# Performance work log

Measured on AMD Instinct MI355X. Metric: run time of the kernel, lower is better.

Reference implementation:

```python
import jax, jax.numpy as jnp
import numpy as np

B, T, D, H = 4, 2048, 1024, 16
DK = D // H
LN_EPS = 1e-5


def setup_inputs() -> dict:
    key = jax.random.key(0)
    ks = jax.random.split(key, 12)
    s = 1.0 / np.sqrt(D)
    inp = {
        'x': jax.random.normal(ks[0], (B, T, D), jnp.float32),
        'Wq': jax.random.normal(ks[1], (D, D), jnp.float32) * s,
        'bq': jnp.zeros((D,), jnp.float32),
        'Wk': jax.random.normal(ks[2], (D, D), jnp.float32) * s,
        'bk': jnp.zeros((D,), jnp.float32),
        'Wv': jax.random.normal(ks[3], (D, D), jnp.float32) * s,
        'bv': jnp.zeros((D,), jnp.float32),
        'Wo': jax.random.normal(ks[4], (D, D), jnp.float32) * s,
        'bo': jnp.zeros((D,), jnp.float32),
        'ln_g': jnp.ones((D,), jnp.float32),
        'ln_b': jnp.zeros((D,), jnp.float32),
    }
    return inp


def reference(x, Wq, bq, Wk, bk, Wv, bv, Wo, bo, ln_g, ln_b):
    b, t, d = x.shape
    scale = jnp.sqrt(jnp.asarray(DK, x.dtype))
    # QKV projections -> [b, h, t, dk]
    q = (x @ Wq + bq).reshape(b, t, H, DK).transpose(0, 2, 1, 3)
    k = (x @ Wk + bk).reshape(b, t, H, DK).transpose(0, 2, 1, 3)
    v = (x @ Wv + bv).reshape(b, t, H, DK).transpose(0, 2, 1, 3)
    scores = jnp.einsum('bhqd,bhkd->bhqk', q, k) / scale  # [b,h,t,t]
    mask = jnp.tril(jnp.ones((t, t), x.dtype))[None, None]  # [1,1,t,t]
    neg = jnp.finfo(x.dtype).min
    scores = jnp.where(mask == 0, neg, scores)
    attn = jax.nn.softmax(scores, axis=-1)
    # mask-renormalize (as in the torch module)
    attn = attn * mask
    denom = attn.sum(-1, keepdims=True)
    attn = jnp.where(denom > 0, attn / denom, jnp.zeros_like(attn))
    ctx = jnp.einsum('bhqk,bhkd->bhqd', attn, v)  # [b,h,t,dk]
    ctx = ctx.transpose(0, 2, 1, 3).reshape(b, t, d)
    out = ctx @ Wo + bo
    y = out + x  # residual
    mu = y.mean(-1, keepdims=True)
    var = ((y - mu) ** 2).mean(-1, keepdims=True)
    return (y - mu) / jnp.sqrt(var + LN_EPS) * ln_g + ln_b
```

## Files before the change

### kernel.cpp

```cpp
#include <hip/hip_runtime.h>


using u16 = unsigned short;
using u32 = unsigned int;
typedef _Float16 f16x8 __attribute__((ext_vector_type(8)));
typedef __fp16 h16x2 __attribute__((ext_vector_type(2)));
typedef float f32x4 __attribute__((ext_vector_type(4)));
typedef unsigned short u16x8 __attribute__((ext_vector_type(8)));
typedef unsigned short u16x4 __attribute__((ext_vector_type(4)));

template <bool B> struct BoolTag { static constexpr bool v = B; };

__device__ inline u16 f2h_bits(float f) {
    _Float16 h = (_Float16)f;
    return __builtin_bit_cast(u16, h);
}
__device__ inline float h2f(u16 u) {
    return (float)__builtin_bit_cast(_Float16, u);
}

__device__ __forceinline__ void gload16(const void* g, void* l) {
    __builtin_amdgcn_global_load_lds(
        (const __attribute__((address_space(1))) void*)g,
        (__attribute__((address_space(3))) void*)l, 16, 0, 0);
}

__global__ __launch_bounds__(256) void convert_kernel(
    const float* __restrict__ x, u16* __restrict__ xb,
    const float* __restrict__ W0, const float* __restrict__ W1,
    const float* __restrict__ W2, const float* __restrict__ W3,
    u16* __restrict__ Wt) {
    __shared__ float ts[64][68];
    const int bid = blockIdx.x, tid = threadIdx.x;
    if (bid < 4096) {
        size_t i = ((size_t)bid * 256 + tid) * 8;
        float4 a = *(const float4*)(x + i);
        float4 b = *(const float4*)(x + i + 4);
        u16x8 o;
        o[0] = f2h_bits(a.x); o[1] = f2h_bits(a.y); o[2] = f2h_bits(a.z); o[3] = f2h_bits(a.w);
        o[4] = f2h_bits(b.x); o[5] = f2h_bits(b.y); o[6] = f2h_bits(b.z); o[7] = f2h_bits(b.w);
        *(u16x8*)(xb + i) = o;
        return;
    }
    const int wb = bid - 4096;
    const int z = wb >> 8, rem = wb & 255;
    const float* W = z == 0 ? W0 : (z == 1 ? W1 : (z == 2 ? W2 : W3));
    u16* Wo = Wt + (size_t)z * 1048576;
    const int k0 = (rem >> 4) * 64, n0 = (rem & 15) * 64;
    const int rr = tid >> 3, c = tid & 7;
#pragma unroll
    for (int p = 0; p < 2; p++) {
        int k = p * 32 + rr;
        float4 u = *(const float4*)(W + (size_t)(k0 + k) * 1024 + n0 + c * 8);
        float4 w = *(const float4*)(W + (size_t)(k0 + k) * 1024 + n0 + c * 8 + 4);
        *(float4*)&ts[k][c * 8] = u;
        *(float4*)&ts[k][c * 8 + 4] = w;
    }
    __syncthreads();
#pragma unroll
    for (int p = 0; p < 2; p++) {
        int n = p * 32 + rr;
        u16 o[8];
#pragma unroll
        for (int j = 0; j < 8; j++) o[j] = f2h_bits(ts[c * 8 + j][n]);
        *(u16x8*)(Wo + (size_t)(n0 + n) * 1024 + k0 + c * 8) = *(u16x8*)o;
    }
}

template <int MODE>
__global__ __launch_bounds__(512) void gemm256_kernel(
    const u16* __restrict__ A, const u16* __restrict__ Wt,
    const float* __restrict__ b0, const float* __restrict__ b1,
    const float* __restrict__ b2, u16* __restrict__ qo, u16* __restrict__ ko,
    u16* __restrict__ vt) {
    constexpr int NBY = (MODE == 0) ? 12 : 4;
    __shared__ u16 As[3][128 * 64];
    __shared__ u16 Bs[3][256 * 64];

    const int bid = blockIdx.x;
    const int cpx = (MODE == 0) ? 96 : 32;
    const int swz = (bid & 7) * cpx + (bid >> 3);
    const int bx = swz / NBY, by = swz % NBY;
    const size_t row0 = (size_t)bx * 128;
    const size_t col0 = (size_t)by * 256;

    const int tid = threadIdx.x, lane = tid & 63;
    const int wid = tid >> 6, wm = wid >> 2, wn = wid & 3;
    const int l15 = lane & 15, lg = lane >> 4;
    const int rr = tid >> 3, c8 = tid & 7;
    const int scw = (c8 ^ (rr & 7)) * 8;

    f32x4 acc[4][4] = {};

    auto stage_half = [&](int kt, u16* dA, u16* dB, int h) {
        const int k0 = kt * 64;
        if (h == 0) {
            gload16(A + (row0 + rr) * 1024 + k0 + scw, dA + tid * 8);
            gload16(Wt + (col0 + rr) * 1024 + k0 + scw, dB + tid * 8);
            gload16(Wt + (col0 + 64 + rr) * 1024 + k0 + scw, dB + (512 + tid) * 8);
        } else {
            gload16(A + (row0 + 64 + rr) * 1024 + k0 + scw, dA + (512 + tid) * 8);
            gload16(Wt + (col0 + 128 + rr) * 1024 + k0 + scw, dB + (1024 + tid) * 8);
            gload16(Wt + (col0 + 192 + rr) * 1024 + k0 + scw, dB + (1536 + tid) * 8);
        }
    };

    auto ldops = [&](const u16* bA, const u16* bB, int kcv, f16x8* Af, f16x8* Bf) {
        const int swo = ((kcv * 4 + lg) ^ (l15 & 7)) * 8;
#pragma unroll
        for (int n = 0; n < 4; n++)
            Bf[n] = *(const f16x8*)(bB + (wn * 64 + n * 16 + l15) * 64 + swo);
#pragma unroll
        for (int m = 0; m < 4; m++)
            Af[m] = *(const f16x8*)(bA + (wm * 64 + m * 16 + l15) * 64 + swo);
    };

    auto domfma = [&](const f16x8* Af, const f16x8* Bf) {
        __builtin_amdgcn_s_setprio(1);
#pragma unroll
        for (int m = 0; m < 4; m++)
#pragma unroll
            for (int n = 0; n < 4; n++)
                acc[m][n] = __builtin_amdgcn_mfma_f32_16x16x32_f16(
                    Af[m], Bf[n], acc[m][n], 0, 0, 0);
        __builtin_amdgcn_s_setprio(0);
    };

    u16 *pA = &As[0][0], *pnA = &As[1][0], *ppA = &As[2][0];
    u16 *pB = &Bs[0][0], *pnB = &Bs[1][0], *ppB = &Bs[2][0];

    stage_half(0, pA, pB, 0);
    stage_half(0, pA, pB, 1);
    stage_half(1, pnA, pnB, 0);
    stage_half(1, pnA, pnB, 1);
    asm volatile("s_waitcnt vmcnt(6)" ::: "memory");
    __builtin_amdgcn_sched_barrier(0);
    __builtin_amdgcn_s_barrier();

#pragma unroll 1
    for (int t = 0; t < 16; t++) {
        f16x8 af[4], bf[4];
        ldops(pA, pB, 0, af, bf);
        if (t < 14) stage_half(t + 2, ppA, ppB, 0);
        __builtin_amdgcn_sched_barrier(0);
        __builtin_amdgcn_s_barrier();
        asm volatile("s_waitcnt lgkmcnt(0)" ::: "memory");
        __builtin_amdgcn_sched_barrier(0);
        domfma(af, bf);
        __builtin_amdgcn_sched_barrier(0);
        __builtin_amdgcn_s_barrier();
        ldops(pA, pB, 1, af, bf);
        if (t < 14) stage_half(t + 2, ppA, ppB, 1);
        if (t < 14)       asm volatile("s_waitcnt vmcnt(6)" ::: "memory");
        else if (t == 14) asm volatile("s_waitcnt vmcnt(0)" ::: "memory");
        __builtin_amdgcn_sched_barrier(0);
        __builtin_amdgcn_s_barrier();
        asm volatile("s_waitcnt lgkmcnt(0)" ::: "memory");
        __builtin_amdgcn_sched_barrier(0);
        domfma(af, bf);
        __builtin_amdgcn_sched_barrier(0);
        if (t < 15) {
            __builtin_amdgcn_s_barrier();
            u16* tp;
            tp = pA; pA = pnA; pnA = ppA; ppA = tp;
            tp = pB; pB = pnB; pnB = ppB; ppB = tp;
        }
    }

    if (MODE == 0) {
        const int zsel = by >> 2;
        if (zsel < 2) {
            u16* ob = zsel == 0 ? qo : ko;
            const float* bias = zsel == 0 ? b0 : b1;
            const float qs = zsel == 0 ? 0.18033688f : 1.0f;
#pragma unroll
            for (int m = 0; m < 4; m++) {
#pragma unroll
                for (int n = 0; n < 4; n++) {
                    size_t col = col0 + wn * 64 + n * 16 + l15;
                    size_t colz = col & 1023;
                    float bb = bias[colz];
#pragma unroll
                    for (int r = 0; r < 4; r++) {
                        size_t row = row0 + wm * 64 + m * 16 + lg * 4 + r;
                        ob[row * 1024 + colz] = f2h_bits((acc[m][n][r] + bb) * qs);
                    }
                }
            }
        } else {
            u16* TL = &Bs[0][0];
            __syncthreads();
#pragma unroll
            for (int m = 0; m < 4; m++) {
#pragma unroll
                for (int n = 0; n < 4; n++) {
                    int cl = wn * 64 + n * 16 + l15;
                    float bb = b2[(col0 & 1023) + cl];
#pragma unroll
                    for (int r = 0; r < 4; r++) {
                        int rl = wm * 64 + m * 16 + lg * 4 + r;
                        TL[cl * 134 + rl] = f2h_bits(acc[m][n][r] + bb);
                    }
                }
            }
            __syncthreads();
            const int vrl = tid >> 1, th = tid & 1;
            size_t vrow = (row0 >> 11) * 1024 + (col0 & 1023) + vrl;
            const int t0loc = (int)(row0 & 2047) + th * 64;
#pragma unroll
            for (int j = 0; j < 8; j++)
                *(u16x8*)(vt + vrow * 2048 + t0loc + j * 8) =
                    *(const u16x8*)(TL + vrl * 134 + th * 64 + j * 8);
        }
    } else {
        u16* yo = qo;
        const u16* xres = ko;
#pragma unroll
        for (int m = 0; m < 4; m++) {
#pragma unroll
            for (int n = 0; n < 4; n++) {
                size_t col = col0 + wn * 64 + n * 16 + l15;
                float bb = b0[col];
#pragma unroll
                for (int r = 0; r < 4; r++) {
                    size_t row = row0 + wm * 64 + m * 16 + lg * 4 + r;
                    size_t idx = row * 1024 + col;
                    yo[idx] = f2h_bits(acc[m][n][r] + bb + h2f(xres[idx]));
                }
            }
        }
    }
}

__global__ __launch_bounds__(512) void attn_kernel(const u16* __restrict__ Q,
                                                   const u16* __restrict__ Kb,
                                                   const u16* __restrict__ Vt,
                                                   u16* __restrict__ ctx) {
    __shared__ u16 Ks[2][64 * 64];
    __shared__ u16 Vs[2][64 * 64];
    __shared__ u16 Ps[8][2][16][72];

    const int bh = blockIdx.x;
    const int b = bh >> 4, h = bh & 15;
    const int qb = 7 - (int)blockIdx.y;
    const int tid = threadIdx.x, lane = tid & 63, wid = tid >> 6;
    const int l15 = lane & 15, lg = lane >> 4;
    const int q0w = qb * 256 + wid * 32;
    const int send = qb * 256;

    const int rr = tid >> 3, c8 = tid & 7;
    const int scw = (c8 ^ (rr & 7)) * 8;
    const size_t kbase = ((size_t)b * 2048) * 1024 + h * 64 + scw;
    const size_t vbase = ((size_t)bh * 64 + rr) * 2048 + scw;

    f16x8 qv[2][2];
#pragma unroll
    for (int qf = 0; qf < 2; qf++) {
        size_t qoff = ((size_t)b * 2048 + q0w + qf * 16 + l15) * 1024 + h * 64 + lg * 8;
        qv[qf][0] = *(const f16x8*)(Q + qoff);
        qv[qf][1] = *(const f16x8*)(Q + qoff + 32);
    }

    const int swk0 = (lg ^ (l15 & 7)) * 8;
    const int swk1 = ((4 + lg) ^ (l15 & 7)) * 8;
    u16* Pw0 = &Ps[wid][0][0][0] + l15 * 72;
    u16* Pw1 = &Ps[wid][1][0][0] + l15 * 72;

    const h16x2 one2 = {(__fp16)1.0f, (__fp16)1.0f};

    f32x4 acc[2][4] = {};
    float psum[2] = {0.0f, 0.0f};

    auto stage = [&](int s, int bf) {
        gload16(Kb + kbase + (size_t)(s + rr) * 1024, Ks[bf] + tid * 8);
        gload16(Vt + vbase + s, Vs[bf] + tid * 8);
    };

    auto body = [&](int s, int bf, auto maskc) {
        constexpr bool MASK = decltype(maskc)::v;
#pragma unroll
        for (int c = 0; c < 4; c++) {
            const u16* kp = Ks[bf] + (c * 16 + l15) * 64;
            f16x8 kf0 = *(const f16x8*)(kp + swk0);
            f16x8 kf1 = *(const f16x8*)(kp + swk1);
#pragma unroll
            for (int qf = 0; qf < 2; qf++) {
                f32x4 z = {};
                z = __builtin_amdgcn_mfma_f32_16x16x32_f16(kf0, qv[qf][0], z, 0, 0, 0);
                z = __builtin_amdgcn_mfma_f32_16x16x32_f16(kf1, qv[qf][1], z, 0, 0, 0);
                float p0 = __builtin_amdgcn_exp2f(z[0]);
                float p1 = __builtin_amdgcn_exp2f(z[1]);
                float p2 = __builtin_amdgcn_exp2f(z[2]);
                float p3 = __builtin_amdgcn_exp2f(z[3]);
                if (MASK) {
                    int kk = s + c * 16 + lg * 4;
                    int qq = q0w + qf * 16 + l15;
                    p0 = (kk + 0 <= qq) ? p0 : 0.0f;
                    p1 = (kk + 1 <= qq) ? p1 : 0.0f;
                    p2 = (kk + 2 <= qq) ? p2 : 0.0f;
                    p3 = (kk + 3 <= qq) ? p3 : 0.0f;
                }
                h16x2 w0 = __builtin_amdgcn_cvt_pkrtz(p0, p1);
                h16x2 w1 = __builtin_amdgcn_cvt_pkrtz(p2, p3);
                psum[qf] = __builtin_amdgcn_fdot2(w0, one2, psum[qf], false);
                psum[qf] = __builtin_amdgcn_fdot2(w1, one2, psum[qf], false);
                uint2 w;
                w.x = __builtin_bit_cast(u32, w0);
                w.y = __builtin_bit_cast(u32, w1);
                *(uint2*)((qf ? Pw1 : Pw0) + c * 16 + lg * 4) = w;
            }
        }
        f16x8 pa0[2], pa1[2];
#pragma unroll
        for (int qf = 0; qf < 2; qf++) {
            const u16* Pw = qf ? Pw1 : Pw0;
            pa0[qf] = *(const f16x8*)(Pw + lg * 8);
            pa1[qf] = *(const f16x8*)(Pw + 32 + lg * 8);
        }
#pragma unroll
        for (int dt = 0; dt < 4; dt++) {
            const u16* vp = Vs[bf] + (dt * 16 + l15) * 64;
            f16x8 vf0 = *(const f16x8*)(vp + swk0);
            f16x8 vf1 = *(const f16x8*)(vp + swk1);
#pragma unroll
            for (int qf = 0; qf < 2; qf++) {
                acc[qf][dt] =
                    __builtin_amdgcn_mfma_f32_16x16x32_f16(pa0[qf], vf0, acc[qf][dt], 0, 0, 0);
                acc[qf][dt] =
                    __builtin_amdgcn_mfma_f32_16x16x32_f16(pa1[qf], vf1, acc[qf][dt], 0, 0, 0);
            }
        }
    };

    stage(0, 0);
    stage(64, 1);
    asm volatile("s_waitcnt vmcnt(2)" ::: "memory");
    __builtin_amdgcn_sched_barrier(0);
    __builtin_amdgcn_s_barrier();

    int cur = 0;
#pragma unroll 1
    for (int s = 0; s < send; s += 64) {
        body(s, cur, BoolTag<false>{});
        __builtin_amdgcn_sched_barrier(0);
        __builtin_amdgcn_s_barrier();
        stage(s + 128, cur);
        asm volatile("s_waitcnt vmcnt(2)" ::: "memory");
        __builtin_amdgcn_sched_barrier(0);
        __builtin_amdgcn_s_barrier();
        cur ^= 1;
    }
#pragma unroll 1
    for (int j = 0; j < 4; j++) {
        if (wid >= 2 * j) body(send + 64 * j, cur, BoolTag<true>{});
        __builtin_amdgcn_sched_barrier(0);
        __builtin_amdgcn_s_barrier();
        if (j < 2) {
            stage(send + 64 * (j + 2), cur);
            asm volatile("s_waitcnt vmcnt(2)" ::: "memory");
        } else if (j == 2) {
            asm volatile("s_waitcnt vmcnt(0)" ::: "memory");
        }
        __builtin_amdgcn_sched_barrier(0);
        __builtin_amdgcn_s_barrier();
        cur ^= 1;
    }

#pragma unroll
    for (int qf = 0; qf < 2; qf++) {
        psum[qf] += __shfl_xor(psum[qf], 16);
        psum[qf] += __shfl_xor(psum[qf], 32);
    }
#pragma unroll
    for (int qf = 0; qf < 2; qf++) {
        float inv = 1.0f / psum[qf];
#pragma unroll
        for (int r = 0; r < 4; r++) {
            float ir = __shfl(inv, lg * 4 + r);
            size_t row = (size_t)b * 2048 + q0w + qf * 16 + lg * 4 + r;
#pragma unroll
            for (int dt = 0; dt < 4; dt++)
                ctx[row * 1024 + h * 64 + dt * 16 + l15] = f2h_bits(acc[qf][dt][r] * ir);
        }
    }
}

__global__ __launch_bounds__(256) void ln_kernel(const u16* __restrict__ y,
                                                 const float* __restrict__ g,
                                                 const float* __restrict__ bb,
                                                 float* __restrict__ out) {
    const int r = blockIdx.x, tid = threadIdx.x;
    u16x4 v4 = *(const u16x4*)(y + (size_t)r * 1024 + tid * 4);
    float vx = h2f(v4[0]), vy = h2f(v4[1]), vz = h2f(v4[2]), vw = h2f(v4[3]);
    float s = vx + vy + vz + vw;
    float sq = vx * vx + vy * vy + vz * vz + vw * vw;
#pragma unroll
    for (int ofs = 1; ofs < 64; ofs <<= 1) {
        s += __shfl_xor(s, ofs);
        sq += __shfl_xor(sq, ofs);
    }
    __shared__ float as[4], aq[4];
    if ((tid & 63) == 0) { as[tid >> 6] = s; aq[tid >> 6] = sq; }
    __syncthreads();
    s = as[0] + as[1] + as[2] + as[3];
    sq = aq[0] + aq[1] + aq[2] + aq[3];
    float mu = s * (1.0f / 1024.0f);
    float var = sq * (1.0f / 1024.0f) - mu * mu;
    float rstd = rsqrtf(var + 1e-5f);
    float4 gv = *(const float4*)(g + tid * 4);
    float4 bv = *(const float4*)(bb + tid * 4);
    float4 o4;
    o4.x = (vx - mu) * rstd * gv.x + bv.x;
    o4.y = (vy - mu) * rstd * gv.y + bv.y;
    o4.z = (vz - mu) * rstd * gv.z + bv.z;
    o4.w = (vw - mu) * rstd * gv.w + bv.w;
    *(float4*)(out + (size_t)r * 1024 + tid * 4) = o4;
}

extern "C" void kernel_launch(void* const* d_in, const int* in_sizes, int n_in,
                              void* d_out, int out_size, void* d_ws, size_t ws_size,
                              hipStream_t stream) {
    const float* x  = (const float*)d_in[0];
    const float* Wq = (const float*)d_in[1];
    const float* bq = (const float*)d_in[2];
    const float* Wk = (const float*)d_in[3];
    const float* bk = (const float*)d_in[4];
    const float* Wv = (const float*)d_in[5];
    const float* bv = (const float*)d_in[6];
    const float* Wo = (const float*)d_in[7];
    const float* bo = (const float*)d_in[8];
    const float* lg = (const float*)d_in[9];
    const float* lb = (const float*)d_in[10];
    float* out = (float*)d_out;

    char* ws = (char*)d_ws;
    u16* xb = (u16*)(ws + 0);
    u16* wt = (u16*)(ws + 16777216);
    u16* q  = (u16*)(ws + 25165824);
    u16* k  = (u16*)(ws + 41943040);
    u16* vt = (u16*)(ws + 75497472);
    u16* cx = (u16*)(ws + 92274688);
    u16* y16 = (u16*)(ws + 109051904);

    convert_kernel<<<5120, 256, 0, stream>>>(x, xb, Wq, Wk, Wv, Wo, wt);

    gemm256_kernel<0><<<768, 512, 0, stream>>>(xb, wt, bq, bk, bv, q, k, vt);
    attn_kernel<<<dim3(64, 8), 512, 0, stream>>>(q, k, vt, cx);
    gemm256_kernel<1><<<256, 512, 0, stream>>>(cx, wt + 3145728, bo, nullptr,
                                               nullptr, y16, xb, nullptr);
    ln_kernel<<<8192, 256, 0, stream>>>(y16, lg, lb, out);
}
```

Baseline: 172.7 us.

## Double attention KV tile to 128 and shuffle P via permlane swaps

The attention kernel now stages 128-key K/V tiles per iteration instead of 64, which halves the number of barrier-separated steps. The P probability tile is moved from the accumulator layout to the MFMA A-operand layout with permlane32/permlane16 swaps in registers, replacing the LDS scratch write and read-back. The grid is flattened and remapped so heavy and light causal query blocks interleave, and s_setprio raises wave priority around the PV MFMAs. In exchange it uses more registers and LDS per block, and the diagonal masked tail now runs at 128-key granularity.

```diff
diff --git a/kernel.cpp b/kernel.cpp
--- a/kernel.cpp
+++ b/kernel.cpp
@@ -8,6 +8,7 @@
 typedef float f32x4 __attribute__((ext_vector_type(4)));
 typedef unsigned short u16x8 __attribute__((ext_vector_type(8)));
 typedef unsigned short u16x4 __attribute__((ext_vector_type(4)));
+typedef unsigned int u32x4 __attribute__((ext_vector_type(4)));
 
 template <bool B> struct BoolTag { static constexpr bool v = B; };
 
@@ -236,13 +237,14 @@
                                                    const u16* __restrict__ Kb,
                                                    const u16* __restrict__ Vt,
                                                    u16* __restrict__ ctx) {
-    __shared__ u16 Ks[2][64 * 64];
-    __shared__ u16 Vs[2][64 * 64];
-    __shared__ u16 Ps[8][2][16][72];
-
-    const int bh = blockIdx.x;
+    __shared__ u16 Ks[2][128 * 64];
+    __shared__ u16 Vs[2][64 * 128];
+
+    const int i = (int)blockIdx.x;
+    const int bh = i & 63;
+    const int sel = (i >> 6) & 3;
+    const int qb = (i < 256) ? (7 - sel) : sel;
     const int b = bh >> 4, h = bh & 15;
-    const int qb = 7 - (int)blockIdx.y;
     const int tid = threadIdx.x, lane = tid & 63, wid = tid >> 6;
     const int l15 = lane & 15, lg = lane >> 4;
     const int q0w = qb * 256 + wid * 32;
@@ -250,8 +252,11 @@
 
     const int rr = tid >> 3, c8 = tid & 7;
     const int scw = (c8 ^ (rr & 7)) * 8;
+    const int vr = tid >> 4, vc = tid & 15;
+    const int scv = (vc ^ (vr & 15)) * 8;
     const size_t kbase = ((size_t)b * 2048) * 1024 + h * 64 + scw;
-    const size_t vbase = ((size_t)bh * 64 + rr) * 2048 + scw;
+    const size_t vbase0 = ((size_t)bh * 64 + vr) * 2048 + scv;
+    const size_t vbase1 = ((size_t)bh * 64 + vr + 32) * 2048 + scv;
 
     f16x8 qv[2][2];
 #pragma unroll
@@ -263,8 +268,6 @@
 
     const int swk0 = (lg ^ (l15 & 7)) * 8;
     const int swk1 = ((4 + lg) ^ (l15 & 7)) * 8;
-    u16* Pw0 = &Ps[wid][0][0][0] + l15 * 72;
-    u16* Pw1 = &Ps[wid][1][0][0] + l15 * 72;
 
     const h16x2 one2 = {(__fp16)1.0f, (__fp16)1.0f};
 
@@ -273,13 +276,16 @@
 
     auto stage = [&](int s, int bf) {
         gload16(Kb + kbase + (size_t)(s + rr) * 1024, Ks[bf] + tid * 8);
-        gload16(Vt + vbase + s, Vs[bf] + tid * 8);
+        gload16(Kb + kbase + (size_t)(s + rr + 64) * 1024, Ks[bf] + (512 + tid) * 8);
+        gload16(Vt + vbase0 + s, Vs[bf] + tid * 8);
+        gload16(Vt + vbase1 + s, Vs[bf] + (512 + tid) * 8);
     };
 
     auto body = [&](int s, int bf, auto maskc) {
         constexpr bool MASK = decltype(maskc)::v;
-#pragma unroll
-        for (int c = 0; c < 4; c++) {
+        u32 W[2][8][2];
+#pragma unroll
+        for (int c = 0; c < 8; c++) {
             const u16* kp = Ks[bf] + (c * 16 + l15) * 64;
             f16x8 kf0 = *(const f16x8*)(kp + swk0);
             f16x8 kf1 = *(const f16x8*)(kp + swk1);
@@ -304,67 +310,75 @@
                 h16x2 w1 = __builtin_amdgcn_cvt_pkrtz(p2, p3);
                 psum[qf] = __builtin_amdgcn_fdot2(w0, one2, psum[qf], false);
                 psum[qf] = __builtin_amdgcn_fdot2(w1, one2, psum[qf], false);
-                uint2 w;
-                w.x = __builtin_bit_cast(u32, w0);
-                w.y = __builtin_bit_cast(u32, w1);
-                *(uint2*)((qf ? Pw1 : Pw0) + c * 16 + lg * 4) = w;
-            }
-        }
-        f16x8 pa0[2], pa1[2];
+                W[qf][c][0] = __builtin_bit_cast(u32, w0);
+                W[qf][c][1] = __builtin_bit_cast(u32, w1);
+            }
+        }
+        f16x8 pa0[2][2], pa1[2][2];
 #pragma unroll
         for (int qf = 0; qf < 2; qf++) {
-            const u16* Pw = qf ? Pw1 : Pw0;
-            pa0[qf] = *(const f16x8*)(Pw + lg * 8);
-            pa1[qf] = *(const f16x8*)(Pw + 32 + lg * 8);
-        }
+#pragma unroll
+            for (int hf = 0; hf < 2; hf++) {
+                const int c0 = hf * 4;
+                auto sA = __builtin_amdgcn_permlane32_swap(W[qf][c0][0], W[qf][c0 + 1][0], false, false);
+                auto tA = __builtin_amdgcn_permlane16_swap(sA[0], sA[1], false, false);
+                auto sB = __builtin_amdgcn_permlane32_swap(W[qf][c0][1], W[qf][c0 + 1][1], false, false);
+                auto tB = __builtin_amdgcn_permlane16_swap(sB[0], sB[1], false, false);
+                u32x4 v0 = {tA[0], tB[0], tA[1], tB[1]};
+                pa0[qf][hf] = __builtin_bit_cast(f16x8, v0);
+                auto sC = __builtin_amdgcn_permlane32_swap(W[qf][c0 + 2][0], W[qf][c0 + 3][0], false, false);
+                auto tC = __builtin_amdgcn_permlane16_swap(sC[0], sC[1], false, false);
+                auto sD = __builtin_amdgcn_permlane32_swap(W[qf][c0 + 2][1], W[qf][c0 + 3][1], false, false);
+                auto tD = __builtin_amdgcn_permlane16_swap(sD[0], sD[1], false, false);
+                u32x4 v1 = {tC[0], tD[0], tC[1], tD[1]};
+                pa1[qf][hf] = __builtin_bit_cast(f16x8, v1);
+            }
+        }
+        __builtin_amdgcn_s_setprio(1);
 #pragma unroll
         for (int dt = 0; dt < 4; dt++) {
-            const u16* vp = Vs[bf] + (dt * 16 + l15) * 64;
-            f16x8 vf0 = *(const f16x8*)(vp + swk0);
-            f16x8 vf1 = *(const f16x8*)(vp + swk1);
-#pragma unroll
-            for (int qf = 0; qf < 2; qf++) {
-                acc[qf][dt] =
-                    __builtin_amdgcn_mfma_f32_16x16x32_f16(pa0[qf], vf0, acc[qf][dt], 0, 0, 0);
-                acc[qf][dt] =
-                    __builtin_amdgcn_mfma_f32_16x16x32_f16(pa1[qf], vf1, acc[qf][dt], 0, 0, 0);
-            }
-        }
+            const u16* vp = Vs[bf] + (dt * 16 + l15) * 128;
+#pragma unroll
+            for (int hf = 0; hf < 2; hf++) {
+                f16x8 vf0 = *(const f16x8*)(vp + ((hf * 8 + lg) ^ l15) * 8);
+                f16x8 vf1 = *(const f16x8*)(vp + ((hf * 8 + 4 + lg) ^ l15) * 8);
+#pragma unroll
+                for (int qf = 0; qf < 2; qf++) {
+                    acc[qf][dt] = __builtin_amdgcn_mfma_f32_16x16x32_f16(
+                        pa0[qf][hf], vf0, acc[qf][dt], 0, 0, 0);
+                    acc[qf][dt] = __builtin_amdgcn_mfma_f32_16x16x32_f16(
+                        pa1[qf][hf], vf1, acc[qf][dt], 0, 0, 0);
+                }
+            }
+        }
+        __builtin_amdgcn_s_setprio(0);
     };
 
     stage(0, 0);
-    stage(64, 1);
-    asm volatile("s_waitcnt vmcnt(2)" ::: "memory");
+    stage(128, 1);
+    asm volatile("s_waitcnt vmcnt(4)" ::: "memory");
     __builtin_amdgcn_sched_barrier(0);
     __builtin_amdgcn_s_barrier();
 
     int cur = 0;
 #pragma unroll 1
-    for (int s = 0; s < send; s += 64) {
+    for (int s = 0; s < send; s += 128) {
         body(s, cur, BoolTag<false>{});
         __builtin_amdgcn_sched_barrier(0);
         __builtin_amdgcn_s_barrier();
-        stage(s + 128, cur);
-        asm volatile("s_waitcnt vmcnt(2)" ::: "memory");
+        stage(s + 256, cur);
+        asm volatile("s_waitcnt vmcnt(4)" ::: "memory");
         __builtin_amdgcn_sched_barrier(0);
         __builtin_amdgcn_s_barrier();
         cur ^= 1;
     }
-#pragma unroll 1
-    for (int j = 0; j < 4; j++) {
-        if (wid >= 2 * j) body(send + 64 * j, cur, BoolTag<true>{});
-        __builtin_amdgcn_sched_barrier(0);
-        __builtin_amdgcn_s_barrier();
-        if (j < 2) {
-            stage(send + 64 * (j + 2), cur);
-            asm volatile("s_waitcnt vmcnt(2)" ::: "memory");
-        } else if (j == 2) {
-            asm volatile("s_waitcnt vmcnt(0)" ::: "memory");
-        }
-        __builtin_amdgcn_sched_barrier(0);
-        __builtin_amdgcn_s_barrier();
-        cur ^= 1;
-    }
+    body(send, cur, BoolTag<true>{});
+    __builtin_amdgcn_sched_barrier(0);
+    __builtin_amdgcn_s_barrier();
+    asm volatile("s_waitcnt vmcnt(0)" ::: "memory");
+    __builtin_amdgcn_sched_barrier(0);
+    __builtin_amdgcn_s_barrier();
+    if (wid >= 4) body(send + 128, cur ^ 1, BoolTag<true>{});
 
 #pragma unroll
     for (int qf = 0; qf < 2; qf++) {
@@ -445,7 +459,7 @@
     convert_kernel<<<5120, 256, 0, stream>>>(x, xb, Wq, Wk, Wv, Wo, wt);
 
     gemm256_kernel<0><<<768, 512, 0, stream>>>(xb, wt, bq, bk, bv, q, k, vt);
-    attn_kernel<<<dim3(64, 8), 512, 0, stream>>>(q, k, vt, cx);
+    attn_kernel<<<512, 512, 0, stream>>>(q, k, vt, cx);
     gemm256_kernel<1><<<256, 512, 0, stream>>>(cx, wt + 3145728, bo, nullptr,
                                                nullptr, y16, xb, nullptr);
     ln_kernel<<<8192, 256, 0, stream>>>(y16, lg, lb, out);
```

Result: faster. 167.7 us (median of 3 runs) (-2.9%).
